# Kernel tuning notes

Measured on AMD Instinct MI355X. Metric: run time of the kernel, lower is better.

The kernel has to match this reference:

```python
import jax, jax.numpy as jnp
import numpy as np

D_MODEL, D_FF = 1024, 4096
B, T = 4, 2048
K = 614  # int(d_ff * 0.15)


def setup_inputs() -> dict:
    key = jax.random.key(0)
    k1, k2, k3, k4 = jax.random.split(key, 4)
    s_in = 1.0 / np.sqrt(D_MODEL)
    s_ff = 1.0 / np.sqrt(D_FF)
    x = jax.random.normal(k1, (B, T, D_MODEL), jnp.float32)
    # torch nn.Linear default init: U(-1/sqrt(fan_in), 1/sqrt(fan_in)); weight shape [out, in]
    W1 = jax.random.uniform(k2, (D_FF, D_MODEL), jnp.float32, -s_in, s_in)
    W2 = jax.random.uniform(k3, (D_FF, D_MODEL), jnp.float32, -s_in, s_in)
    Wo = jax.random.uniform(k4, (D_MODEL, D_FF), jnp.float32, -s_ff, s_ff)
    return {"x": x, "W1": W1, "W2": W2, "Wo": Wo, "k": K}


def reference(x, W1, W2, Wo, k):
    gate = jnp.einsum('btd,fd->btf', x, W2)                 # [B,T,D_FF]
    act = jax.nn.silu(jnp.einsum('btd,fd->btf', x, W1))     # [B,T,D_FF]
    Bx, Tx, Dff = act.shape
    flat = act.reshape(Bx * Tx, Dff)
    _, topk_idx = jax.lax.top_k(flat, k)                    # [N, k]
    rows = jnp.arange(Bx * Tx)[:, None]
    mask = jnp.zeros_like(flat).at[rows, topk_idx].set(1.0).reshape(act.shape)
    sparse_act = act * mask                                  # eval-mode exact masking
    return jnp.einsum('btf,df->btd', sparse_act * gate, Wo)  # [B,T,D_MODEL]
```

## Files before the change

### kernel.cpp

```cpp
#include <hip/hip_runtime.h>
#include <stdint.h>

#define DEV __device__ __forceinline__

using f32x4  = __attribute__((ext_vector_type(4))) float;
using bf16x8 = __attribute__((ext_vector_type(8))) short;
typedef unsigned short u16;
typedef unsigned int   u32;

typedef const __attribute__((address_space(1))) void* gptr_t;
typedef __attribute__((address_space(3))) void*       lptr_t;

DEV u16 f2bf(float f) {
  union { float f; u32 u; } v; v.f = f;
  u32 lsb = (v.u >> 16) & 1u;
  v.u += 0x7fffu + lsb;
  return (u16)(v.u >> 16);
}
DEV float bf2f(u16 h) {
  union { u32 u; float f; } v; v.u = ((u32)h) << 16;
  return v.f;
}
DEV void async16(void* lds, const void* g) {
  __builtin_amdgcn_global_load_lds((gptr_t)(uintptr_t)g,
                                   (lptr_t)(u32)(uintptr_t)lds, 16, 0, 0);
}
DEV u32 fkey(float v) {
  u32 u = __float_as_uint(v);
  return u ^ ((u & 0x80000000u) ? 0xFFFFFFFFu : 0x80000000u);
}
DEV float unfkey(u32 key) {
  const u32 ub = (key & 0x80000000u) ? (key ^ 0x80000000u) : ~key;
  return __uint_as_float(ub);
}

__global__ __launch_bounds__(256) void split1_kernel(const float* __restrict__ src,
                                                     u16* __restrict__ hi, int n) {
  int i = blockIdx.x * 256 + threadIdx.x;
  if (i >= n) return;
  hi[i] = f2bf(src[i]);
}
__global__ __launch_bounds__(256) void split2_kernel(const float* __restrict__ src,
                                                     u16* __restrict__ hi, u16* __restrict__ lo, int n) {
  int i = blockIdx.x * 256 + threadIdx.x;
  if (i >= n) return;
  float v = src[i];
  u16 h = f2bf(v);
  hi[i] = h;
  lo[i] = f2bf(v - bf2f(h));
}

DEV void swz_block(int& bx, int& by) {
  const int gx = gridDim.x, nwg = gx * gridDim.y;
  const int lid = by * gx + bx;
  const int cpx = nwg >> 3;
  const int swz = (lid & 7) * cpx + (lid >> 3);
  bx = swz % gx; by = swz / gx;
}

template<int K, int NSEG, bool OUTBF16>
__global__ __launch_bounds__(512, 2) void gemm8p_kernel(
    const u16* __restrict__ A0, const u16* __restrict__ A1, const u16* __restrict__ A2,
    const u16* __restrict__ B0, const u16* __restrict__ B1, const u16* __restrict__ B2,
    void* __restrict__ Cout, int N)
{
  __shared__ u16 smem[65536];

  const int tid  = threadIdx.x;
  const int lane = tid & 63;
  const int wid  = tid >> 6;
  const int wm = wid >> 2, wn = wid & 3;
  int bx = blockIdx.x, by = blockIdx.y;
  swz_block(bx, by);
  const int m0 = by * 256, n0 = bx * 256;
  constexpr int TPS    = K >> 6;
  constexpr int nTiles = NSEG * TPS;
  constexpr int nIter  = nTiles / 2;

  f32x4 acc[8][4] = {};
  bf16x8 afr[4][2], bfr[2][2];

  auto stageHT = [&](int ab, int buf, int half, int ktile) {
    const int kt  = ktile < nTiles ? ktile : nTiles - 1;
    const int seg = kt / TPS;
    const int k0  = (kt - seg * TPS) << 6;
    const u16* __restrict__ src =
        ab ? (seg == 0 ? B0 : seg == 1 ? B1 : B2)
           : (seg == 0 ? A0 : seg == 1 ? A1 : A2);
    const int g0 = (ab ? n0 : m0) + half * 128;
    const int baseu = ((buf * 2 + ab) * 2 + half) * 8192;
#pragma unroll
    for (int L = 0; L < 2; ++L) {
      const int s = L * 512 + tid;
      const int r = s >> 3, cs = s & 7;
      const int csg = cs ^ (r & 7);
      async16(smem + baseu + (L * 512 + (tid & ~63)) * 8,
              src + (size_t)(g0 + r) * K + k0 + csg * 8);
    }
  };
  auto ldA = [&](int buf, int mi, int ks) -> bf16x8 {
    const int rA = wm * 128 + mi * 16 + (lane & 15);
    const int h = rA >> 7, rl = rA & 127;
    const int cs = (ks * 4 + (lane >> 4)) ^ (rl & 7);
    return *(const bf16x8*)&smem[((buf * 2 + 0) * 2 + h) * 8192 + rl * 64 + cs * 8];
  };
  auto ldB = [&](int buf, int ni, int ks) -> bf16x8 {
    const int rB = wn * 64 + ni * 16 + (lane & 15);
    const int h = rB >> 7, rl = rB & 127;
    const int cs = (ks * 4 + (lane >> 4)) ^ (rl & 7);
    return *(const bf16x8*)&smem[((buf * 2 + 1) * 2 + h) * 8192 + rl * 64 + cs * 8];
  };

  stageHT(0, 0, 0, 0); stageHT(0, 0, 1, 0);
  stageHT(1, 0, 0, 0); stageHT(1, 0, 1, 0);
  asm volatile("s_waitcnt vmcnt(0)" ::: "memory");
  __builtin_amdgcn_sched_barrier(0);
  __builtin_amdgcn_s_barrier();
  __builtin_amdgcn_sched_barrier(0);

  for (int i = 0; i < nIter; ++i) {
    const int t2 = 2 * i;
#pragma unroll
    for (int p = 0; p < 8; ++p) {
      const int pm = p & 3, bufC = p >> 2;
      const int miB = (pm >> 1) * 4, niB = (pm & 1) * 2;
      if ((pm & 1) == 0) {
#pragma unroll
        for (int m = 0; m < 4; ++m)
#pragma unroll
          for (int ks = 0; ks < 2; ++ks)
            afr[m][ks] = ldA(bufC, miB + m, ks);
      }
#pragma unroll
      for (int n = 0; n < 2; ++n)
#pragma unroll
        for (int ks = 0; ks < 2; ++ks)
          bfr[n][ks] = ldB(bufC, niB + n, ks);
      if (p == 0)      { stageHT(0, 1, 0, t2 + 1); stageHT(0, 1, 1, t2 + 1); }
      else if (p == 1) { stageHT(1, 1, 0, t2 + 1); stageHT(1, 1, 1, t2 + 1); }
      else if (p == 4) { stageHT(0, 0, 0, t2 + 2); stageHT(0, 0, 1, t2 + 2); }
      else if (p == 5) { stageHT(1, 0, 0, t2 + 2); stageHT(1, 0, 1, t2 + 2); }
      __builtin_amdgcn_sched_barrier(0);
      __builtin_amdgcn_s_barrier();
      __builtin_amdgcn_sched_barrier(0);
      __builtin_amdgcn_s_setprio(1);
#pragma unroll
      for (int m = 0; m < 4; ++m)
#pragma unroll
        for (int n = 0; n < 2; ++n)
#pragma unroll
          for (int ks = 0; ks < 2; ++ks)
            acc[miB + m][niB + n] = __builtin_amdgcn_mfma_f32_16x16x32_bf16(
                afr[m][ks], bfr[n][ks], acc[miB + m][niB + n], 0, 0, 0);
      __builtin_amdgcn_s_setprio(0);
      if (pm == 3)
        asm volatile("s_waitcnt vmcnt(0)" ::: "memory");
      __builtin_amdgcn_sched_barrier(0);
      __builtin_amdgcn_s_barrier();
      __builtin_amdgcn_sched_barrier(0);
    }
  }
  asm volatile("s_waitcnt vmcnt(0)" ::: "memory");

#pragma unroll
  for (int mi = 0; mi < 8; ++mi) {
    const int rb = m0 + wm * 128 + mi * 16 + (lane >> 4) * 4;
#pragma unroll
    for (int ni = 0; ni < 4; ++ni) {
      const int col = n0 + wn * 64 + ni * 16 + (lane & 15);
#pragma unroll
      for (int r2 = 0; r2 < 4; ++r2) {
        if constexpr (OUTBF16)
          ((u16*)Cout)[(size_t)(rb + r2) * N + col] = f2bf(acc[mi][ni][r2]);
        else
          ((float*)Cout)[(size_t)(rb + r2) * N + col] = acc[mi][ni][r2];
      }
    }
  }
}

template<int BK>
__global__ __launch_bounds__(256) void gemm_bt(
    const u16* __restrict__ A, const u16* __restrict__ B,
    float* __restrict__ C, int N, int K)
{
  constexpr int TILE = 128 * BK;
  __shared__ u16 smem[2 * TILE];
  u16* sA = smem;
  u16* sB = smem + TILE;

  const int tid  = threadIdx.x;
  const int lane = tid & 63;
  const int wave = tid >> 6;
  const int wr = wave >> 1, wc = wave & 1;
  int bx = blockIdx.x, by = blockIdx.y;
  swz_block(bx, by);
  const int m0 = by * 128, n0 = bx * 128;

  f32x4 acc[4][4] = {};
  constexpr int SPR   = BK / 8;
  constexpr int ITERS = (128 * SPR) / 256;

  for (int k0 = 0; k0 < K; k0 += BK) {
#pragma unroll
    for (int i = 0; i < ITERS; ++i) {
      const int slot = i * 256 + tid;
      const int r = slot / SPR, cc = slot % SPR;
      const int uni = (i * 256 + wave * 64) * 8;
      async16(sA + uni, A + (size_t)(m0 + r) * K + k0 + cc * 8);
      async16(sB + uni, B + (size_t)(n0 + r) * K + k0 + cc * 8);
    }
    __syncthreads();

#pragma unroll
    for (int ks = 0; ks < BK / 32; ++ks) {
      const int kb = ks * 32 + (lane >> 4) * 8;
      bf16x8 a[4], b[4];
#pragma unroll
      for (int i = 0; i < 4; ++i) {
        a[i] = *(const bf16x8*)&sA[(wr * 64 + i * 16 + (lane & 15)) * BK + kb];
        b[i] = *(const bf16x8*)&sB[(wc * 64 + i * 16 + (lane & 15)) * BK + kb];
      }
#pragma unroll
      for (int mi = 0; mi < 4; ++mi)
#pragma unroll
        for (int ni = 0; ni < 4; ++ni)
          acc[mi][ni] = __builtin_amdgcn_mfma_f32_16x16x32_bf16(a[mi], b[ni], acc[mi][ni], 0, 0, 0);
    }
    __syncthreads();
  }

#pragma unroll
  for (int mi = 0; mi < 4; ++mi) {
    const int rbase = m0 + wr * 64 + mi * 16 + (lane >> 4) * 4;
#pragma unroll
    for (int ni = 0; ni < 4; ++ni) {
      const int col = n0 + wc * 64 + ni * 16 + (lane & 15);
#pragma unroll
      for (int r2 = 0; r2 < 4; ++r2)
        C[(size_t)(rbase + r2) * N + col] = acc[mi][ni][r2];
    }
  }
}

__global__ __launch_bounds__(256) void select9_kernel(
    const float* __restrict__ z, const u16* __restrict__ g,
    const float* __restrict__ xin, const float* __restrict__ W1,
    u16* __restrict__ sbuf, const int* __restrict__ kptr)
{
  const int row = blockIdx.x, tid = threadIdx.x;
  const int lane = tid & 63, wave = tid >> 6;
  const int k = *kptr;

  __shared__ float xrow[1024];
  __shared__ float sact[4096];
  __shared__ unsigned char flag[4096];
  __shared__ int wsum[4];
  __shared__ int s_nb;
  __shared__ int band_idx[256];
  __shared__ u32 band_key[256];
  __shared__ float band_act[256];

  const float* zrow = z + (size_t)row * 4096;
  const u16*   grow = g + (size_t)row * 4096;

  float zreg[16];
#pragma unroll
  for (int q = 0; q < 4; ++q) {
    const float4 v = *(const float4*)&zrow[q * 1024 + tid * 4];
    zreg[q * 4 + 0] = v.x; zreg[q * 4 + 1] = v.y;
    zreg[q * 4 + 2] = v.z; zreg[q * 4 + 3] = v.w;
  }
  *(float4*)&xrow[tid * 4] = *(const float4*)&xin[(size_t)row * 1024 + tid * 4];
  *(u32*)&flag[tid * 4] = 0u;
  *(u32*)&flag[1024 + tid * 4] = 0u;
  *(u32*)&flag[2048 + tid * 4] = 0u;
  *(u32*)&flag[3072 + tid * 4] = 0u;
  if (tid == 0) s_nb = 0;
  __syncthreads();

  u32 prefix = 0;
  for (int step = 0; step < 20; ++step) {
    const u32 c = prefix | (1u << (31 - step));
    const float zc = unfkey(c);
    int cnt = 0;
#pragma unroll
    for (int i = 0; i < 16; ++i) cnt += (zreg[i] >= zc) ? 1 : 0;
    for (int off = 32; off; off >>= 1) cnt += __shfl_xor(cnt, off);
    if (lane == 0) wsum[wave] = cnt;
    __syncthreads();
    const int tot = wsum[0] + wsum[1] + wsum[2] + wsum[3];
    if (tot >= k) prefix = c;
    __syncthreads();
  }
  const float tau = unfkey(prefix);
  const float BANDW = 8e-4f;
  const float thi = tau + BANDW, tlo = tau - BANDW;

  int cntD = 0;
#pragma unroll
  for (int q = 0; q < 4; ++q)
#pragma unroll
    for (int j = 0; j < 4; ++j) {
      const int f = q * 1024 + tid * 4 + j;
      const float zv = zreg[q * 4 + j];
      if (zv > thi) { flag[f] = 1; ++cntD; }
      else if (zv >= tlo) {
        const int p = atomicAdd(&s_nb, 1);
        if (p < 256) band_idx[p] = f;
      }
    }
  for (int off = 32; off; off >>= 1) cntD += __shfl_xor(cntD, off);
  if (lane == 0) wsum[wave] = cntD;
  __syncthreads();
  const int D = wsum[0] + wsum[1] + wsum[2] + wsum[3];
  const int nb = (s_nb < 256) ? s_nb : 256;
  const int need = k - D;

  {
    const int gi = tid >> 2, l = tid & 3;
    const int wl = lane & ~3;
    for (int i = gi; i < nb; i += 64) {
      const int f = band_idx[i];
      const float* wr = W1 + (size_t)f * 1024;
      float v = 0.f;
#pragma unroll 8
      for (int b = 0; b < 1024; b += 16) {
        float t = __fadd_rn(__fmul_rn(xrow[b + 12 + l], wr[b + 12 + l]), v);
        t = __fadd_rn(__fmul_rn(xrow[b + 8 + l],  wr[b + 8 + l]),  t);
        t = __fadd_rn(__fmul_rn(xrow[b + 4 + l],  wr[b + 4 + l]),  t);
        v = __fadd_rn(__fmul_rn(xrow[b + 0 + l],  wr[b + 0 + l]),  t);
      }
      const float c0 = __shfl(v, wl + 0);
      const float c1 = __shfl(v, wl + 1);
      const float c2 = __shfl(v, wl + 2);
      const float c3 = __shfl(v, wl + 3);
      if (l == 0) {
        const float zrep = __fadd_rn(__fadd_rn(c0, c1), __fadd_rn(c2, c3));
        const double zd = (double)zrep;
        const float a = (float)(zd / (1.0 + exp(-zd)));
        band_act[i] = a;
        band_key[i] = fkey(a);
      }
    }
  }
  __syncthreads();

  for (int i = tid; i < nb; i += 256) {
    const u32 ki = band_key[i];
    const int fi = band_idx[i];
    int rank = 0;
    for (int j = 0; j < nb; ++j) {
      const u32 kj = band_key[j];
      rank += (kj > ki || (kj == ki && band_idx[j] < fi)) ? 1 : 0;
    }
    if (rank < need) { flag[fi] = 2; sact[fi] = band_act[i]; }
  }
  __syncthreads();

  u16* srow = sbuf + (size_t)row * 4096;
#pragma unroll
  for (int q = 0; q < 4; ++q) {
    const int f0 = q * 1024 + tid * 4;
    const ushort4 gu = *(const ushort4*)&grow[f0];
    const float gvv[4] = { bf2f(gu.x), bf2f(gu.y), bf2f(gu.z), bf2f(gu.w) };
    const u32 fl = *(const u32*)&flag[f0];
    u16 out[4];
#pragma unroll
    for (int j = 0; j < 4; ++j) {
      const u32 fj = (fl >> (8 * j)) & 0xFF;
      float sval = 0.f;
      if (fj == 2) {
        sval = sact[f0 + j] * gvv[j];
      } else if (fj == 1) {
        const float zz = zreg[q * 4 + j];
        sval = (zz / (1.f + expf(-zz))) * gvv[j];
      }
      out[j] = f2bf(sval);
    }
    *(ushort4*)&srow[f0] = make_ushort4(out[0], out[1], out[2], out[3]);
  }
}

extern "C" void kernel_launch(void* const* d_in, const int* in_sizes, int n_in,
                              void* d_out, int out_size, void* d_ws, size_t ws_size,
                              hipStream_t stream)
{
  const float* x  = (const float*)d_in[0];
  const float* W1 = (const float*)d_in[1];
  const float* W2 = (const float*)d_in[2];
  const float* Wo = (const float*)d_in[3];
  const int* kptr = (const int*)d_in[4];

  const int DM = 1024, DF = 4096;
  const int M = in_sizes[0] / DM;
  const size_t nX = (size_t)M * DM, nW = (size_t)DF * DM, nWo = (size_t)DM * DF;

  char* w = (char*)d_ws;
  u16* x_hi  = (u16*)w;  w += nX * 2;
  u16* x_lo  = (u16*)w;  w += nX * 2;
  u16* W1_hi = (u16*)w;  w += nW * 2;
  u16* W1_lo = (u16*)w;  w += nW * 2;
  u16* W2_hi = (u16*)w;  w += nW * 2;
  u16* Wo_hi = (u16*)w;  w += nWo * 2;
  const size_t fixed_bytes = (size_t)(w - (char*)d_ws);

  int nch = 1;
  while (nch < 64) {
    const size_t per = (size_t)(M / nch) * DF * 8;
    if (fixed_bytes + per <= ws_size) break;
    nch *= 2;
  }
  const int Mc = M / nch;

  float* zbuf = (float*)w;
  u16*   gbuf = (u16*)(w + (size_t)Mc * DF * 4);
  u16*   sbuf = (u16*)(w + (size_t)Mc * DF * 6);

  split2_kernel<<<dim3((int)((nX + 255) / 256)), 256, 0, stream>>>(x, x_hi, x_lo, (int)nX);
  split2_kernel<<<dim3((int)((nW + 255) / 256)), 256, 0, stream>>>(W1, W1_hi, W1_lo, (int)nW);
  split1_kernel<<<dim3((int)((nW + 255) / 256)), 256, 0, stream>>>(W2, W2_hi, (int)nW);
  split1_kernel<<<dim3((int)((nWo + 255) / 256)), 256, 0, stream>>>(Wo, Wo_hi, (int)nWo);

  for (int ch = 0; ch < nch; ++ch) {
    const size_t ro = (size_t)ch * Mc;
    gemm8p_kernel<1024, 3, false><<<dim3(DF / 256, Mc / 256), 512, 0, stream>>>(
        x_hi + ro * DM, x_hi + ro * DM, x_lo + ro * DM,
        W1_hi, W1_lo, W1_hi, zbuf, DF);
    gemm8p_kernel<1024, 1, true><<<dim3(DF / 256, Mc / 256), 512, 0, stream>>>(
        x_hi + ro * DM, x_hi + ro * DM, x_hi + ro * DM,
        W2_hi, W2_hi, W2_hi, gbuf, DF);
    select9_kernel<<<dim3(Mc), 256, 0, stream>>>(
        zbuf, gbuf, x + ro * DM, W1, sbuf, kptr);
    gemm_bt<64><<<dim3(DM / 128, Mc / 128), 256, 0, stream>>>(
        sbuf, Wo_hi, (float*)d_out + ro * DM, DM, DF);
  }
}
```

Measured before the change: 647.4 us.

## Switch gemm8p to 32x32x16 MFMA, fuse split kernels, reuse gate buffer in place

The main GEMM kernel moves from 16x16x32 to 32x32x16 bf16 MFMA instructions. This reorganises the accumulators into f32x16 tiles and changes the LDS fragment addressing and epilogue row mapping to match, aiming for fewer LDS reads per MFMA and higher matrix-core throughput. The four fp32-to-bf16 split launches become one fused launch. select9 now writes the sparse product back into the gate buffer in place, which shrinks the workspace per chunk and may allow fewer chunks. The threshold bisection also grows from 20 to 22 steps, which adds a little select cost and narrows the threshold search.

```diff
diff --git a/kernel.cpp b/kernel.cpp
--- a/kernel.cpp
+++ b/kernel.cpp
@@ -4,6 +4,7 @@
 #define DEV __device__ __forceinline__
 
 using f32x4  = __attribute__((ext_vector_type(4))) float;
+using f32x16 = __attribute__((ext_vector_type(16))) float;
 using bf16x8 = __attribute__((ext_vector_type(8))) short;
 typedef unsigned short u16;
 typedef unsigned int   u32;
@@ -34,20 +35,33 @@
   return __uint_as_float(ub);
 }
 
-__global__ __launch_bounds__(256) void split1_kernel(const float* __restrict__ src,
-                                                     u16* __restrict__ hi, int n) {
-  int i = blockIdx.x * 256 + threadIdx.x;
-  if (i >= n) return;
-  hi[i] = f2bf(src[i]);
-}
-__global__ __launch_bounds__(256) void split2_kernel(const float* __restrict__ src,
-                                                     u16* __restrict__ hi, u16* __restrict__ lo, int n) {
-  int i = blockIdx.x * 256 + threadIdx.x;
-  if (i >= n) return;
-  float v = src[i];
-  u16 h = f2bf(v);
-  hi[i] = h;
-  lo[i] = f2bf(v - bf2f(h));
+__global__ __launch_bounds__(256) void splitall_kernel(
+    const float* __restrict__ x,  const float* __restrict__ W1,
+    const float* __restrict__ W2, const float* __restrict__ Wo,
+    u16* __restrict__ x_hi, u16* __restrict__ x_lo,
+    u16* __restrict__ W1h,  u16* __restrict__ W1l,
+    u16* __restrict__ W2h,  u16* __restrict__ Woh,
+    int nX, int nW, int nWo)
+{
+  const int i = blockIdx.x * 256 + threadIdx.x;
+  const int total = nX + 2 * nW + nWo;
+  if (i >= total) return;
+  if (i < nX) {
+    const float v = x[i];
+    const u16 h = f2bf(v);
+    x_hi[i] = h; x_lo[i] = f2bf(v - bf2f(h));
+  } else if (i < nX + nW) {
+    const int j = i - nX;
+    const float v = W1[j];
+    const u16 h = f2bf(v);
+    W1h[j] = h; W1l[j] = f2bf(v - bf2f(h));
+  } else if (i < nX + 2 * nW) {
+    const int j = i - nX - nW;
+    W2h[j] = f2bf(W2[j]);
+  } else {
+    const int j = i - nX - 2 * nW;
+    Woh[j] = f2bf(Wo[j]);
+  }
 }
 
 DEV void swz_block(int& bx, int& by) {
@@ -77,8 +91,8 @@
   constexpr int nTiles = NSEG * TPS;
   constexpr int nIter  = nTiles / 2;
 
-  f32x4 acc[8][4] = {};
-  bf16x8 afr[4][2], bfr[2][2];
+  f32x16 acc[4][2] = {};
+  bf16x8 afr[2][4], bfr[4];
 
   auto stageHT = [&](int ab, int buf, int half, int ktile) {
     const int kt  = ktile < nTiles ? ktile : nTiles - 1;
@@ -99,15 +113,15 @@
     }
   };
   auto ldA = [&](int buf, int mi, int ks) -> bf16x8 {
-    const int rA = wm * 128 + mi * 16 + (lane & 15);
+    const int rA = wm * 128 + mi * 32 + (lane & 31);
     const int h = rA >> 7, rl = rA & 127;
-    const int cs = (ks * 4 + (lane >> 4)) ^ (rl & 7);
+    const int cs = (ks * 2 + (lane >> 5)) ^ (rl & 7);
     return *(const bf16x8*)&smem[((buf * 2 + 0) * 2 + h) * 8192 + rl * 64 + cs * 8];
   };
   auto ldB = [&](int buf, int ni, int ks) -> bf16x8 {
-    const int rB = wn * 64 + ni * 16 + (lane & 15);
+    const int rB = wn * 64 + ni * 32 + (lane & 31);
     const int h = rB >> 7, rl = rB & 127;
-    const int cs = (ks * 4 + (lane >> 4)) ^ (rl & 7);
+    const int cs = (ks * 2 + (lane >> 5)) ^ (rl & 7);
     return *(const bf16x8*)&smem[((buf * 2 + 1) * 2 + h) * 8192 + rl * 64 + cs * 8];
   };
 
@@ -123,19 +137,17 @@
 #pragma unroll
     for (int p = 0; p < 8; ++p) {
       const int pm = p & 3, bufC = p >> 2;
-      const int miB = (pm >> 1) * 4, niB = (pm & 1) * 2;
+      const int mh = pm >> 1, nn = pm & 1;
       if ((pm & 1) == 0) {
 #pragma unroll
-        for (int m = 0; m < 4; ++m)
-#pragma unroll
-          for (int ks = 0; ks < 2; ++ks)
-            afr[m][ks] = ldA(bufC, miB + m, ks);
-      }
-#pragma unroll
-      for (int n = 0; n < 2; ++n)
-#pragma unroll
-        for (int ks = 0; ks < 2; ++ks)
-          bfr[n][ks] = ldB(bufC, niB + n, ks);
+        for (int m2 = 0; m2 < 2; ++m2)
+#pragma unroll
+          for (int ks = 0; ks < 4; ++ks)
+            afr[m2][ks] = ldA(bufC, mh * 2 + m2, ks);
+      }
+#pragma unroll
+      for (int ks = 0; ks < 4; ++ks)
+        bfr[ks] = ldB(bufC, nn, ks);
       if (p == 0)      { stageHT(0, 1, 0, t2 + 1); stageHT(0, 1, 1, t2 + 1); }
       else if (p == 1) { stageHT(1, 1, 0, t2 + 1); stageHT(1, 1, 1, t2 + 1); }
       else if (p == 4) { stageHT(0, 0, 0, t2 + 2); stageHT(0, 0, 1, t2 + 2); }
@@ -145,13 +157,11 @@
       __builtin_amdgcn_sched_barrier(0);
       __builtin_amdgcn_s_setprio(1);
 #pragma unroll
-      for (int m = 0; m < 4; ++m)
-#pragma unroll
-        for (int n = 0; n < 2; ++n)
-#pragma unroll
-          for (int ks = 0; ks < 2; ++ks)
-            acc[miB + m][niB + n] = __builtin_amdgcn_mfma_f32_16x16x32_bf16(
-                afr[m][ks], bfr[n][ks], acc[miB + m][niB + n], 0, 0, 0);
+      for (int m2 = 0; m2 < 2; ++m2)
+#pragma unroll
+        for (int ks = 0; ks < 4; ++ks)
+          acc[mh * 2 + m2][nn] = __builtin_amdgcn_mfma_f32_32x32x16_bf16(
+              afr[m2][ks], bfr[ks], acc[mh * 2 + m2][nn], 0, 0, 0);
       __builtin_amdgcn_s_setprio(0);
       if (pm == 3)
         asm volatile("s_waitcnt vmcnt(0)" ::: "memory");
@@ -163,17 +173,18 @@
   asm volatile("s_waitcnt vmcnt(0)" ::: "memory");
 
 #pragma unroll
-  for (int mi = 0; mi < 8; ++mi) {
-    const int rb = m0 + wm * 128 + mi * 16 + (lane >> 4) * 4;
-#pragma unroll
-    for (int ni = 0; ni < 4; ++ni) {
-      const int col = n0 + wn * 64 + ni * 16 + (lane & 15);
-#pragma unroll
-      for (int r2 = 0; r2 < 4; ++r2) {
+  for (int mi = 0; mi < 4; ++mi) {
+#pragma unroll
+    for (int ni = 0; ni < 2; ++ni) {
+      const f32x16 v = acc[mi][ni];
+      const int col = n0 + wn * 64 + ni * 32 + (lane & 31);
+#pragma unroll
+      for (int r = 0; r < 16; ++r) {
+        const int row = m0 + wm * 128 + mi * 32 + (r & 3) + 8 * (r >> 2) + 4 * (lane >> 5);
         if constexpr (OUTBF16)
-          ((u16*)Cout)[(size_t)(rb + r2) * N + col] = f2bf(acc[mi][ni][r2]);
+          ((u16*)Cout)[(size_t)row * N + col] = f2bf(v[r]);
         else
-          ((float*)Cout)[(size_t)(rb + r2) * N + col] = acc[mi][ni][r2];
+          ((float*)Cout)[(size_t)row * N + col] = v[r];
       }
     }
   }
@@ -244,9 +255,9 @@
 }
 
 __global__ __launch_bounds__(256) void select9_kernel(
-    const float* __restrict__ z, const u16* __restrict__ g,
+    const float* __restrict__ z, u16* __restrict__ gs,
     const float* __restrict__ xin, const float* __restrict__ W1,
-    u16* __restrict__ sbuf, const int* __restrict__ kptr)
+    const int* __restrict__ kptr)
 {
   const int row = blockIdx.x, tid = threadIdx.x;
   const int lane = tid & 63, wave = tid >> 6;
@@ -262,7 +273,7 @@
   __shared__ float band_act[256];
 
   const float* zrow = z + (size_t)row * 4096;
-  const u16*   grow = g + (size_t)row * 4096;
+  u16* gsrow = gs + (size_t)row * 4096;
 
   float zreg[16];
 #pragma unroll
@@ -280,7 +291,7 @@
   __syncthreads();
 
   u32 prefix = 0;
-  for (int step = 0; step < 20; ++step) {
+  for (int step = 0; step < 22; ++step) {
     const u32 c = prefix | (1u << (31 - step));
     const float zc = unfkey(c);
     int cnt = 0;
@@ -358,11 +369,10 @@
   }
   __syncthreads();
 
-  u16* srow = sbuf + (size_t)row * 4096;
 #pragma unroll
   for (int q = 0; q < 4; ++q) {
     const int f0 = q * 1024 + tid * 4;
-    const ushort4 gu = *(const ushort4*)&grow[f0];
+    const ushort4 gu = *(const ushort4*)&gsrow[f0];
     const float gvv[4] = { bf2f(gu.x), bf2f(gu.y), bf2f(gu.z), bf2f(gu.w) };
     const u32 fl = *(const u32*)&flag[f0];
     u16 out[4];
@@ -378,7 +388,7 @@
       }
       out[j] = f2bf(sval);
     }
-    *(ushort4*)&srow[f0] = make_ushort4(out[0], out[1], out[2], out[3]);
+    *(ushort4*)&gsrow[f0] = make_ushort4(out[0], out[1], out[2], out[3]);
   }
 }
 
@@ -407,20 +417,21 @@
 
   int nch = 1;
   while (nch < 64) {
-    const size_t per = (size_t)(M / nch) * DF * 8;
+    const size_t per = (size_t)(M / nch) * DF * 6;
     if (fixed_bytes + per <= ws_size) break;
     nch *= 2;
   }
   const int Mc = M / nch;
 
-  float* zbuf = (float*)w;
-  u16*   gbuf = (u16*)(w + (size_t)Mc * DF * 4);
-  u16*   sbuf = (u16*)(w + (size_t)Mc * DF * 6);
-
-  split2_kernel<<<dim3((int)((nX + 255) / 256)), 256, 0, stream>>>(x, x_hi, x_lo, (int)nX);
-  split2_kernel<<<dim3((int)((nW + 255) / 256)), 256, 0, stream>>>(W1, W1_hi, W1_lo, (int)nW);
-  split1_kernel<<<dim3((int)((nW + 255) / 256)), 256, 0, stream>>>(W2, W2_hi, (int)nW);
-  split1_kernel<<<dim3((int)((nWo + 255) / 256)), 256, 0, stream>>>(Wo, Wo_hi, (int)nWo);
+  float* zbuf  = (float*)w;
+  u16*   gsbuf = (u16*)(w + (size_t)Mc * DF * 4);
+
+  {
+    const long long total = (long long)nX + 2 * (long long)nW + (long long)nWo;
+    splitall_kernel<<<dim3((int)((total + 255) / 256)), 256, 0, stream>>>(
+        x, W1, W2, Wo, x_hi, x_lo, W1_hi, W1_lo, W2_hi, Wo_hi,
+        (int)nX, (int)nW, (int)nWo);
+  }
 
   for (int ch = 0; ch < nch; ++ch) {
     const size_t ro = (size_t)ch * Mc;
@@ -429,10 +440,10 @@
         W1_hi, W1_lo, W1_hi, zbuf, DF);
     gemm8p_kernel<1024, 1, true><<<dim3(DF / 256, Mc / 256), 512, 0, stream>>>(
         x_hi + ro * DM, x_hi + ro * DM, x_hi + ro * DM,
-        W2_hi, W2_hi, W2_hi, gbuf, DF);
+        W2_hi, W2_hi, W2_hi, gsbuf, DF);
     select9_kernel<<<dim3(Mc), 256, 0, stream>>>(
-        zbuf, gbuf, x + ro * DM, W1, sbuf, kptr);
+        zbuf, gsbuf, x + ro * DM, W1, kptr);
     gemm_bt<64><<<dim3(DM / 128, Mc / 128), 256, 0, stream>>>(
-        sbuf, Wo_hi, (float*)d_out + ro * DM, DM, DF);
-  }
-}
+        gsbuf, Wo_hi, (float*)d_out + ro * DM, DM, DF);
+  }
+}
```

After: 718.3 us. +10.9%, slower.
